# Optimization experiments

Measured on AMD Instinct MI355X. Metric: run time of the kernel, lower is better.

The kernel has to match this reference:

```python
import jax, jax.numpy as jnp
import numpy as np

NU, NI, D, H = 200000, 100000, 128, 128
E = 600000

def _segment_mean(vals, seg_ids, num_segments):
    s = jax.ops.segment_sum(vals, seg_ids, num_segments=num_segments)
    cnt = jax.ops.segment_sum(jnp.ones((vals.shape[0],), vals.dtype), seg_ids, num_segments=num_segments)
    return s / jnp.maximum(cnt, 1.0)[:, None]


def setup_inputs() -> dict:
    key = jax.random.key(0)
    ks = jax.random.split(key, 16)
    sc = 1.0 / np.sqrt(D)
    return {
        'x_user': jax.random.normal(ks[0], (NU, D), jnp.float32),
        'x_item': jax.random.normal(ks[1], (NI, D), jnp.float32),
        'edge_src_ui': jax.random.randint(ks[2], (E,), 0, NU),
        'edge_dst_ui': jax.random.randint(ks[3], (E,), 0, NI),
        'edge_src_iu': jax.random.randint(ks[4], (E,), 0, NI),
        'edge_dst_iu': jax.random.randint(ks[5], (E,), 0, NU),
        'Wl_ui': jax.random.normal(ks[6], (D, H), jnp.float32) * sc,
        'bl_ui': jax.random.normal(ks[7], (H,), jnp.float32) * 0.01,
        'Wr_ui': jax.random.normal(ks[8], (D, H), jnp.float32) * sc,
        'Wl_iu': jax.random.normal(ks[9], (D, H), jnp.float32) * sc,
        'bl_iu': jax.random.normal(ks[10], (H,), jnp.float32) * 0.01,
        'Wr_iu': jax.random.normal(ks[11], (D, H), jnp.float32) * sc,
        'W_user': jax.random.normal(ks[12], (H, H), jnp.float32) * sc,
        'b_user': jax.random.normal(ks[13], (H,), jnp.float32) * 0.01,
        'W_item': jax.random.normal(ks[14], (H, H), jnp.float32) * sc,
        'b_item': jax.random.normal(ks[15], (H,), jnp.float32) * 0.01,
    }


def reference(x_user, x_item, edge_src_ui, edge_dst_ui, edge_src_iu, edge_dst_iu,
              Wl_ui, bl_ui, Wr_ui, Wl_iu, bl_iu, Wr_iu,
              W_user, b_user, W_item, b_item):
    # SAGEConv per edge type: out_dst = mean_aggr(x_src[src]) @ Wl + bl + x_dst @ Wr
    agg_item = _segment_mean(x_user[edge_src_ui], edge_dst_ui, NI)   # [NI, D]
    h_item = agg_item @ Wl_ui + bl_ui + x_item @ Wr_ui               # [NI, H]
    agg_user = _segment_mean(x_item[edge_src_iu], edge_dst_iu, NU)   # [NU, D]
    h_user = agg_user @ Wl_iu + bl_iu + x_user @ Wr_iu               # [NU, H]
    # HeteroConv aggr='sum' is trivial here (one edge type per dst node type).
    out_user = jax.nn.relu(h_user @ W_user + b_user)
    out_item = jax.nn.relu(h_item @ W_item + b_item)
    return jnp.concatenate([out_user, out_item], axis=0)  # [NU+NI, H]
```

## Files before the change

kernel.cpp:

```cpp
#include <hip/hip_runtime.h>

#define NUu 200000
#define NIi 100000
#define EE  600000

#define SCAP 768
#define NB_USER 3125
#define NB_ITEM 1563

#define PB_HIST   586
#define PB_W0     1172
#define PB_B0     1428
#define PB_CU0    1429
#define PB_CI0    13929
#define PB_END    20179

typedef short short8 __attribute__((ext_vector_type(8)));
typedef float floatx4 __attribute__((ext_vector_type(4)));

__device__ __forceinline__ unsigned short f2bf(float f) {
  union { float f; unsigned int u; } v; v.f = f;
  unsigned int r = v.u + 0x7FFFu + ((v.u >> 16) & 1u);
  return (unsigned short)(r >> 16);
}
__device__ __forceinline__ float bflo(unsigned int u) { return __uint_as_float(u << 16); }
__device__ __forceinline__ float bfhi(unsigned int u) { return __uint_as_float(u & 0xFFFF0000u); }

__global__ __launch_bounds__(256) void prep(
    const int* __restrict__ edst_iu, int* __restrict__ cnt_user,
    const int* __restrict__ edst_ui, int* __restrict__ cnt_item,
    const float* __restrict__ Wl_iu, const float* __restrict__ Wr_iu,
    const float* __restrict__ Wl_ui, const float* __restrict__ Wr_ui,
    const float* __restrict__ W_user, const float* __restrict__ W_item,
    unsigned short* __restrict__ Wp_user, unsigned short* __restrict__ Wp_item,
    const float* __restrict__ bl_iu, const float* __restrict__ b_user,
    const float* __restrict__ bl_ui, const float* __restrict__ b_item,
    float* __restrict__ bias_user, float* __restrict__ bias_item,
    const float* __restrict__ x_user, const float* __restrict__ x_item,
    unsigned short* __restrict__ xb_user, unsigned short* __restrict__ xb_item)
{
  int b = blockIdx.x, t = threadIdx.x;
  if (b < PB_W0) {
    const int* edst = b < PB_HIST ? edst_iu : edst_ui;
    int* cnt        = b < PB_HIST ? cnt_user : cnt_item;
    int local       = b < PB_HIST ? b : b - PB_HIST;
    int idx = local * 1024 + t * 4;
    if (idx < EE) {
      int4 v = *(const int4*)(edst + idx);
      atomicAdd(&cnt[v.x], 1); atomicAdd(&cnt[v.y], 1);
      atomicAdd(&cnt[v.z], 1); atomicAdd(&cnt[v.w], 1);
    }
  } else if (b < PB_B0) {
    int flat = (b - PB_W0) * 256 + t;
    int h = flat & 127, d = (flat >> 7) & 127, m = flat >> 14;
    const float* A; const float* W; unsigned short* dst; int koff;
    switch (m) {
      case 0:  A = Wl_iu; W = W_user; dst = Wp_user; koff = 0;   break;
      case 1:  A = Wr_iu; W = W_user; dst = Wp_user; koff = 128; break;
      case 2:  A = Wl_ui; W = W_item; dst = Wp_item; koff = 0;   break;
      default: A = Wr_ui; W = W_item; dst = Wp_item; koff = 128; break;
    }
    float acc = 0.f;
    for (int k = 0; k < 128; ++k) acc += A[d * 128 + k] * W[k * 128 + h];
    int kg = koff + d;
    int ks = kg >> 5, quad = (kg >> 3) & 3, j = kg & 7;
    int nt = h >> 4, nlo = h & 15;
    dst[((nt * 8 + ks) * 64 + quad * 16 + nlo) * 8 + j] = f2bf(acc);
  } else if (b == PB_B0) {
    int pair = t >> 7, h = t & 127;
    const float* bl = pair ? bl_ui : bl_iu;
    const float* b2 = pair ? b_item : b_user;
    const float* W  = pair ? W_item : W_user;
    float* o        = pair ? bias_item : bias_user;
    float acc = b2[h];
    for (int k = 0; k < 128; ++k) acc += bl[k] * W[k * 128 + h];
    o[h] = acc;
  } else {
    const float* src; unsigned short* dst; long base;
    if (b < PB_CI0) { src = x_user; dst = xb_user; base = (long)(b - PB_CU0) * 2048 + t * 8; }
    else            { src = x_item; dst = xb_item; base = (long)(b - PB_CI0) * 2048 + t * 8; }
    const float4* p4 = (const float4*)(src + base);
    float4 lo = p4[0], hi = p4[1];
    uint4 p;
    p.x = (unsigned)f2bf(lo.x) | ((unsigned)f2bf(lo.y) << 16);
    p.y = (unsigned)f2bf(lo.z) | ((unsigned)f2bf(lo.w) << 16);
    p.z = (unsigned)f2bf(hi.x) | ((unsigned)f2bf(hi.y) << 16);
    p.w = (unsigned)f2bf(hi.z) | ((unsigned)f2bf(hi.w) << 16);
    *(uint4*)(dst + base) = p;
  }
}

__global__ __launch_bounds__(256) void scan1(
    const int* __restrict__ cnt_u, int* __restrict__ blk_u,
    const int* __restrict__ cnt_i, int* __restrict__ blk_i)
{
  __shared__ int s[256];
  int b = blockIdx.x, t = threadIdx.x;
  const int* cnt; int* blksum; int N;
  if (blockIdx.y == 0) { cnt = cnt_u; blksum = blk_u; N = NUu; }
  else { if (b >= 98) return; cnt = cnt_i; blksum = blk_i; N = NIi; }
  int base = b * 1024 + t * 4;
  int v = 0;
  #pragma unroll
  for (int j = 0; j < 4; ++j) { int i = base + j; if (i < N) v += cnt[i]; }
  s[t] = v; __syncthreads();
  for (int off = 128; off > 0; off >>= 1) {
    if (t < off) s[t] += s[t + off];
    __syncthreads();
  }
  if (t == 0) blksum[b] = s[0];
}

__global__ __launch_bounds__(256) void scan3(
    const int* __restrict__ cnt_u, const int* __restrict__ blks_u,
    int* __restrict__ row_u, int* __restrict__ fil_u,
    const int* __restrict__ cnt_i, const int* __restrict__ blks_i,
    int* __restrict__ row_i, int* __restrict__ fil_i)
{
  __shared__ int s[256];
  int b = blockIdx.x, t = threadIdx.x;
  const int* cnt; const int* blksum; int* rowp; int* fillp; int N; int nblk;
  if (blockIdx.y == 0) { cnt = cnt_u; blksum = blks_u; rowp = row_u; fillp = fil_u; N = NUu; nblk = 196; }
  else { if (b >= 98) return; cnt = cnt_i; blksum = blks_i; rowp = row_i; fillp = fil_i; N = NIi; nblk = 98; }

  int v2 = t < nblk ? blksum[t] : 0;
  s[t] = v2; __syncthreads();
  for (int off = 1; off < 256; off <<= 1) {
    int tmp = t >= off ? s[t - off] : 0;
    __syncthreads();
    s[t] += tmp;
    __syncthreads();
  }
  int blkoffb = (b == 0) ? 0 : s[b - 1];
  __syncthreads();

  int base = b * 1024 + t * 4;
  int v[4]; int sum = 0;
  #pragma unroll
  for (int j = 0; j < 4; ++j) { int i = base + j; v[j] = (i < N) ? cnt[i] : 0; sum += v[j]; }
  s[t] = sum; __syncthreads();
  for (int off = 1; off < 256; off <<= 1) {
    int tmp = t >= off ? s[t - off] : 0;
    __syncthreads();
    s[t] += tmp;
    __syncthreads();
  }
  int ex = s[t] - sum + blkoffb;
  #pragma unroll
  for (int j = 0; j < 4; ++j) {
    int i = base + j;
    if (i < N) { rowp[i] = ex; fillp[i] = ex; ex += v[j]; }
  }
}

__global__ __launch_bounds__(256) void fill2(
    const int* __restrict__ esrc_iu, const int* __restrict__ edst_iu,
    int* __restrict__ fill_user, int* __restrict__ srcs_user,
    const int* __restrict__ esrc_ui, const int* __restrict__ edst_ui,
    int* __restrict__ fill_item, int* __restrict__ srcs_item)
{
  int e = blockIdx.x * 256 + threadIdx.x;
  if (e >= EE) return;
  const int* esrc; const int* edst; int* fillp; int* srcs;
  if (blockIdx.y == 0) { esrc = esrc_iu; edst = edst_iu; fillp = fill_user; srcs = srcs_user; }
  else                 { esrc = esrc_ui; edst = edst_ui; fillp = fill_item; srcs = srcs_item; }
  int d = edst[e];
  int p = atomicAdd(&fillp[d], 1);
  srcs[p] = esrc[e];
}

template<bool BF>
__global__ __launch_bounds__(256, 8) void fused_gemm(
    const void* __restrict__ xu_own, const void* __restrict__ xu_src,
    const int* __restrict__ rowp_u, const int* __restrict__ srcs_u,
    const unsigned short* __restrict__ Wp_u, const float* __restrict__ bias_u,
    const void* __restrict__ xi_own, const void* __restrict__ xi_src,
    const int* __restrict__ rowp_i, const int* __restrict__ srcs_i,
    const unsigned short* __restrict__ Wp_i, const float* __restrict__ bias_i,
    float* __restrict__ out)
{
  __shared__ __align__(16) uint4 ldsA4[1024];
  __shared__ int ldsS[SCAP];
  __shared__ int rb[65];
  int t = threadIdx.x;
  int b = blockIdx.x;

  const void* xown; const void* xsrc; const int* rowp; const int* srcs;
  const unsigned short* Wp; const float* bias; float* outbase; int nvalid; int node0;
  if (b < NB_USER) {
    xown = xu_own; xsrc = xu_src; rowp = rowp_u; srcs = srcs_u;
    Wp = Wp_u; bias = bias_u; outbase = out; nvalid = NUu; node0 = b * 64;
  } else {
    xown = xi_own; xsrc = xi_src; rowp = rowp_i; srcs = srcs_i;
    Wp = Wp_i; bias = bias_i; outbase = out + (size_t)NUu * 128;
    nvalid = NIi; node0 = (b - NB_USER) * 64;
  }

  if (t < 65) {
    int node = node0 + t;
    rb[t] = node < nvalid ? rowp[node] : EE;
  }
  __syncthreads();
  int rs0 = rb[0];
  int W = rb[64] - rs0;
  for (int idx = t; idx < W && idx < SCAP; idx += 256)
    ldsS[idx] = srcs[rs0 + idx];

  #pragma unroll
  for (int i = 0; i < 4; ++i) {
    int oid = t + i * 256;
    int m = oid >> 4;
    int oct = oid & 15;
    int node = node0 + m;
    uint4 p; p.x = 0u; p.y = 0u; p.z = 0u; p.w = 0u;
    if (node < nvalid) {
      if constexpr (BF) {
        p = *(const uint4*)((const unsigned short*)xown + (size_t)node * 128 + oct * 8);
      } else {
        const float4* p4 = (const float4*)((const float*)xown + (size_t)node * 128 + oct * 8);
        float4 lo = p4[0], hi = p4[1];
        p.x = (unsigned)f2bf(lo.x) | ((unsigned)f2bf(lo.y) << 16);
        p.y = (unsigned)f2bf(lo.z) | ((unsigned)f2bf(lo.w) << 16);
        p.z = (unsigned)f2bf(hi.x) | ((unsigned)f2bf(hi.y) << 16);
        p.w = (unsigned)f2bf(hi.z) | ((unsigned)f2bf(hi.w) << 16);
      }
    }
    int ks = oct >> 2, quad = oct & 3;
    int mt = m >> 4, mlo = m & 15;
    ldsA4[(mt * 4 + ks) * 64 + quad * 16 + (mlo ^ (oct & 7))] = p;
  }
  __syncthreads();

  int wave = t >> 6, lane = t & 63;
  int quadr = lane >> 4, mlor = lane & 15;
  floatx4 acc[8];
  #pragma unroll
  for (int i = 0; i < 8; ++i) acc[i] = (floatx4){0.f, 0.f, 0.f, 0.f};
  const short8* A = (const short8*)ldsA4;
  const short8* B = (const short8*)Wp;
  #pragma unroll
  for (int kk = 0; kk < 4; ++kk) {
    short8 af = A[(wave * 4 + kk) * 64 + quadr * 16 + (mlor ^ ((kk * 4 + quadr) & 7))];
    #pragma unroll
    for (int nt = 0; nt < 8; ++nt) {
      short8 bf = B[(nt * 8 + 4 + kk) * 64 + lane];
      acc[nt] = __builtin_amdgcn_mfma_f32_16x16x32_bf16(af, bf, acc[nt], 0, 0, 0);
    }
  }
  __syncthreads();

  #pragma unroll
  for (int i = 0; i < 8; ++i) {
    int oid = t + i * 256;
    int m = oid >> 5;
    int oct = oid & 31;
    int slice = oct & 15;
    int par = oct >> 4;
    int node = node0 + m;
    float a0=0,a1=0,a2=0,a3=0,a4=0,a5=0,a6=0,a7=0;
    int deg = 0;
    if (node < nvalid) {
      int erel = rb[m] - rs0;
      deg = rb[m + 1] - rb[m];
      int k0 = slice * 8;
      int e = par;
      if constexpr (BF) {
        const unsigned short* xs = (const unsigned short*)xsrc;
        for (; e + 2 < deg; e += 4) {
          int q0 = erel + e, q1 = q0 + 2;
          int s0 = (q0 < SCAP) ? ldsS[q0] : srcs[rs0 + q0];
          int s1 = (q1 < SCAP) ? ldsS[q1] : srcs[rs0 + q1];
          uint4 v0 = *(const uint4*)(xs + (size_t)s0 * 128 + k0);
          uint4 v1 = *(const uint4*)(xs + (size_t)s1 * 128 + k0);
          a0 += bflo(v0.x) + bflo(v1.x); a1 += bfhi(v0.x) + bfhi(v1.x);
          a2 += bflo(v0.y) + bflo(v1.y); a3 += bfhi(v0.y) + bfhi(v1.y);
          a4 += bflo(v0.z) + bflo(v1.z); a5 += bfhi(v0.z) + bfhi(v1.z);
          a6 += bflo(v0.w) + bflo(v1.w); a7 += bfhi(v0.w) + bfhi(v1.w);
        }
        if (e < deg) {
          int q = erel + e;
          int s = (q < SCAP) ? ldsS[q] : srcs[rs0 + q];
          uint4 v0 = *(const uint4*)(xs + (size_t)s * 128 + k0);
          a0 += bflo(v0.x); a1 += bfhi(v0.x);
          a2 += bflo(v0.y); a3 += bfhi(v0.y);
          a4 += bflo(v0.z); a5 += bfhi(v0.z);
          a6 += bflo(v0.w); a7 += bfhi(v0.w);
        }
      } else {
        const float* xs = (const float*)xsrc;
        for (; e + 2 < deg; e += 4) {
          int q0 = erel + e, q1 = q0 + 2;
          int s0 = (q0 < SCAP) ? ldsS[q0] : srcs[rs0 + q0];
          int s1 = (q1 < SCAP) ? ldsS[q1] : srcs[rs0 + q1];
          const float4* r0 = (const float4*)(xs + (size_t)s0 * 128 + k0);
          const float4* r1 = (const float4*)(xs + (size_t)s1 * 128 + k0);
          float4 l0 = r0[0], h0 = r0[1];
          float4 l1 = r1[0], h1 = r1[1];
          a0 += l0.x + l1.x; a1 += l0.y + l1.y;
          a2 += l0.z + l1.z; a3 += l0.w + l1.w;
          a4 += h0.x + h1.x; a5 += h0.y + h1.y;
          a6 += h0.z + h1.z; a7 += h0.w + h1.w;
        }
        if (e < deg) {
          int q = erel + e;
          int s = (q < SCAP) ? ldsS[q] : srcs[rs0 + q];
          const float4* r = (const float4*)(xs + (size_t)s * 128 + k0);
          float4 l = r[0], h = r[1];
          a0 += l.x; a1 += l.y; a2 += l.z; a3 += l.w;
          a4 += h.x; a5 += h.y; a6 += h.z; a7 += h.w;
        }
      }
    }
    a0 += __shfl_xor(a0, 16); a1 += __shfl_xor(a1, 16);
    a2 += __shfl_xor(a2, 16); a3 += __shfl_xor(a3, 16);
    a4 += __shfl_xor(a4, 16); a5 += __shfl_xor(a5, 16);
    a6 += __shfl_xor(a6, 16); a7 += __shfl_xor(a7, 16);
    if (par == 0) {
      float sc = deg > 0 ? 1.0f / (float)deg : 0.f;
      uint4 p;
      p.x = (unsigned)f2bf(a0 * sc) | ((unsigned)f2bf(a1 * sc) << 16);
      p.y = (unsigned)f2bf(a2 * sc) | ((unsigned)f2bf(a3 * sc) << 16);
      p.z = (unsigned)f2bf(a4 * sc) | ((unsigned)f2bf(a5 * sc) << 16);
      p.w = (unsigned)f2bf(a6 * sc) | ((unsigned)f2bf(a7 * sc) << 16);
      int ks = slice >> 2, quad = slice & 3;
      int mt = m >> 4, mlo = m & 15;
      ldsA4[(mt * 4 + ks) * 64 + quad * 16 + (mlo ^ (slice & 7))] = p;
    }
  }
  __syncthreads();

  #pragma unroll
  for (int kk = 0; kk < 4; ++kk) {
    short8 af = A[(wave * 4 + kk) * 64 + quadr * 16 + (mlor ^ ((kk * 4 + quadr) & 7))];
    #pragma unroll
    for (int nt = 0; nt < 8; ++nt) {
      short8 bf = B[(nt * 8 + kk) * 64 + lane];
      acc[nt] = __builtin_amdgcn_mfma_f32_16x16x32_bf16(af, bf, acc[nt], 0, 0, 0);
    }
  }

  int col = lane & 15, qrow = (lane >> 4) * 4;
  #pragma unroll
  for (int nt = 0; nt < 8; ++nt) {
    int n = nt * 16 + col;
    float bv = bias[n];
    #pragma unroll
    for (int r2 = 0; r2 < 4; ++r2) {
      int node = node0 + wave * 16 + qrow + r2;
      if (node < nvalid) {
        float v = acc[nt][r2] + bv;
        v = v > 0.f ? v : 0.f;
        __builtin_nontemporal_store(v, &outbase[(size_t)node * 128 + n]);
      }
    }
  }
}

extern "C" void kernel_launch(void* const* d_in, const int* in_sizes, int n_in,
                              void* d_out, int out_size, void* d_ws, size_t ws_size,
                              hipStream_t stream)
{
  const float* x_user = (const float*)d_in[0];
  const float* x_item = (const float*)d_in[1];
  const int* esrc_ui  = (const int*)d_in[2];
  const int* edst_ui  = (const int*)d_in[3];
  const int* esrc_iu  = (const int*)d_in[4];
  const int* edst_iu  = (const int*)d_in[5];
  const float* Wl_ui  = (const float*)d_in[6];
  const float* bl_ui  = (const float*)d_in[7];
  const float* Wr_ui  = (const float*)d_in[8];
  const float* Wl_iu  = (const float*)d_in[9];
  const float* bl_iu  = (const float*)d_in[10];
  const float* Wr_iu  = (const float*)d_in[11];
  const float* W_user = (const float*)d_in[12];
  const float* b_user = (const float*)d_in[13];
  const float* W_item = (const float*)d_in[14];
  const float* b_item = (const float*)d_in[15];
  float* out = (float*)d_out;

  char* ws = (char*)d_ws;
  int* cnt_user  = (int*)(ws + 0);
  int* cnt_item  = (int*)(ws + 800000);
  int* row_user  = (int*)(ws + 1200000);
  int* row_item  = (int*)(ws + 2000000);
  int* fill_user = (int*)(ws + 2400000);
  int* fill_item = (int*)(ws + 3200000);
  int* srcs_user = (int*)(ws + 3600000);
  int* srcs_item = (int*)(ws + 6000000);
  int* blks_user = (int*)(ws + 8400000);
  int* blks_item = (int*)(ws + 8401024);
  unsigned short* Wp_user = (unsigned short*)(ws + 8404224);
  unsigned short* Wp_item = (unsigned short*)(ws + 8469760);
  float* bias_user = (float*)(ws + 8535296);
  float* bias_item = (float*)(ws + 8535808);
  unsigned short* xb_user = (unsigned short*)(ws + 8536320);
  unsigned short* xb_item = (unsigned short*)(ws + 59736320UL);

  const bool bf = ws_size >= 85336320UL;

  hipMemsetAsync(d_ws, 0, 1200000, stream);

  prep<<<bf ? PB_END : PB_CU0, 256, 0, stream>>>(
      edst_iu, cnt_user, edst_ui, cnt_item,
      Wl_iu, Wr_iu, Wl_ui, Wr_ui, W_user, W_item, Wp_user, Wp_item,
      bl_iu, b_user, bl_ui, b_item, bias_user, bias_item,
      x_user, x_item, xb_user, xb_item);

  scan1<<<dim3(196, 2), 256, 0, stream>>>(cnt_user, blks_user, cnt_item, blks_item);
  scan3<<<dim3(196, 2), 256, 0, stream>>>(cnt_user, blks_user, row_user, fill_user,
                                          cnt_item, blks_item, row_item, fill_item);

  const int EB = (EE + 255) / 256;
  fill2<<<dim3(EB, 2), 256, 0, stream>>>(esrc_iu, edst_iu, fill_user, srcs_user,
                                         esrc_ui, edst_ui, fill_item, srcs_item);

  if (bf) {
    fused_gemm<true><<<NB_USER + NB_ITEM, 256, 0, stream>>>(
        xb_user, xb_item, row_user, srcs_user, Wp_user, bias_user,
        xb_item, xb_user, row_item, srcs_item, Wp_item, bias_item, out);
  } else {
    fused_gemm<false><<<NB_USER + NB_ITEM, 256, 0, stream>>>(
        x_user, x_item, row_user, srcs_user, Wp_user, bias_user,
        x_item, x_user, row_item, srcs_item, Wp_item, bias_item, out);
  }
}
```

Baseline: 567.5 us.

## Replace global-atomic CSR build with two-level binned counting sort

Builds the CSR adjacency with a two-level counting sort instead of per-node global atomics. Destination nodes are grouped into bins of 512. Per-block shared-memory histograms are prefix-summed by a small kernel, edges are scattered into bin-ordered temporaries, and a per-bin kernel builds row pointers and the source list using shared-memory atomics. This removes the workspace memset and the contended global atomics in histogram and fill. The cost is an extra kernel, a serial 586-step loop per thread in the 2-block scan kernel, and extra temporary traffic.

Measured after the change: 684.2 us. 1.21x slower.

```diff
diff --git a/kernel.cpp b/kernel.cpp
--- a/kernel.cpp
+++ b/kernel.cpp
@@ -8,12 +8,17 @@
 #define NB_USER 3125
 #define NB_ITEM 1563
 
-#define PB_HIST   586
-#define PB_W0     1172
-#define PB_B0     1428
-#define PB_CU0    1429
-#define PB_CI0    13929
-#define PB_END    20179
+#define EB2 586
+#define NBIN 512
+#define BINS_U 391
+#define BINS_I 196
+
+#define PB_HIST 586
+#define PB_W0   1172
+#define PB_B0   1428
+#define PB_CU0  1429
+#define PB_CI0  13929
+#define PB_END  20179
 
 typedef short short8 __attribute__((ext_vector_type(8)));
 typedef float floatx4 __attribute__((ext_vector_type(4)));
@@ -26,9 +31,9 @@
 __device__ __forceinline__ float bflo(unsigned int u) { return __uint_as_float(u << 16); }
 __device__ __forceinline__ float bfhi(unsigned int u) { return __uint_as_float(u & 0xFFFF0000u); }
 
-__global__ __launch_bounds__(256) void prep(
-    const int* __restrict__ edst_iu, int* __restrict__ cnt_user,
-    const int* __restrict__ edst_ui, int* __restrict__ cnt_item,
+__global__ __launch_bounds__(256) void prep1(
+    const int* __restrict__ edst_iu, int* __restrict__ bh_u,
+    const int* __restrict__ edst_ui, int* __restrict__ bh_i,
     const float* __restrict__ Wl_iu, const float* __restrict__ Wr_iu,
     const float* __restrict__ Wl_ui, const float* __restrict__ Wr_ui,
     const float* __restrict__ W_user, const float* __restrict__ W_item,
@@ -39,20 +44,29 @@
     const float* __restrict__ x_user, const float* __restrict__ x_item,
     unsigned short* __restrict__ xb_user, unsigned short* __restrict__ xb_item)
 {
+  __shared__ int h[NBIN];
   int b = blockIdx.x, t = threadIdx.x;
   if (b < PB_W0) {
-    const int* edst = b < PB_HIST ? edst_iu : edst_ui;
-    int* cnt        = b < PB_HIST ? cnt_user : cnt_item;
-    int local       = b < PB_HIST ? b : b - PB_HIST;
-    int idx = local * 1024 + t * 4;
+    bool uside = b < PB_HIST;
+    const int* ed = uside ? edst_iu : edst_ui;
+    int* bh       = uside ? bh_u : bh_i;
+    int lb        = uside ? b : b - PB_HIST;
+    h[t] = 0; h[t + 256] = 0;
+    __syncthreads();
+    int idx = lb * 1024 + t * 4;
     if (idx < EE) {
-      int4 v = *(const int4*)(edst + idx);
-      atomicAdd(&cnt[v.x], 1); atomicAdd(&cnt[v.y], 1);
-      atomicAdd(&cnt[v.z], 1); atomicAdd(&cnt[v.w], 1);
-    }
+      int4 d = *(const int4*)(ed + idx);
+      atomicAdd(&h[d.x >> 9], 1);
+      atomicAdd(&h[d.y >> 9], 1);
+      atomicAdd(&h[d.z >> 9], 1);
+      atomicAdd(&h[d.w >> 9], 1);
+    }
+    __syncthreads();
+    bh[t * EB2 + lb] = h[t];
+    bh[(t + 256) * EB2 + lb] = h[t + 256];
   } else if (b < PB_B0) {
     int flat = (b - PB_W0) * 256 + t;
-    int h = flat & 127, d = (flat >> 7) & 127, m = flat >> 14;
+    int hh = flat & 127, d = (flat >> 7) & 127, m = flat >> 14;
     const float* A; const float* W; unsigned short* dst; int koff;
     switch (m) {
       case 0:  A = Wl_iu; W = W_user; dst = Wp_user; koff = 0;   break;
@@ -61,20 +75,20 @@
       default: A = Wr_ui; W = W_item; dst = Wp_item; koff = 128; break;
     }
     float acc = 0.f;
-    for (int k = 0; k < 128; ++k) acc += A[d * 128 + k] * W[k * 128 + h];
+    for (int k = 0; k < 128; ++k) acc += A[d * 128 + k] * W[k * 128 + hh];
     int kg = koff + d;
     int ks = kg >> 5, quad = (kg >> 3) & 3, j = kg & 7;
-    int nt = h >> 4, nlo = h & 15;
+    int nt = hh >> 4, nlo = hh & 15;
     dst[((nt * 8 + ks) * 64 + quad * 16 + nlo) * 8 + j] = f2bf(acc);
   } else if (b == PB_B0) {
-    int pair = t >> 7, h = t & 127;
+    int pair = t >> 7, hh = t & 127;
     const float* bl = pair ? bl_ui : bl_iu;
     const float* b2 = pair ? b_item : b_user;
     const float* W  = pair ? W_item : W_user;
     float* o        = pair ? bias_item : bias_user;
-    float acc = b2[h];
-    for (int k = 0; k < 128; ++k) acc += bl[k] * W[k * 128 + h];
-    o[h] = acc;
+    float acc = b2[hh];
+    for (int k = 0; k < 128; ++k) acc += bl[k] * W[k * 128 + hh];
+    o[hh] = acc;
   } else {
     const float* src; unsigned short* dst; long base;
     if (b < PB_CI0) { src = x_user; dst = xb_user; base = (long)(b - PB_CU0) * 2048 + t * 8; }
@@ -90,83 +104,114 @@
   }
 }
 
-__global__ __launch_bounds__(256) void scan1(
-    const int* __restrict__ cnt_u, int* __restrict__ blk_u,
-    const int* __restrict__ cnt_i, int* __restrict__ blk_i)
-{
-  __shared__ int s[256];
+__global__ __launch_bounds__(512) void prep2(
+    int* __restrict__ bh_u, int* __restrict__ bb_u,
+    int* __restrict__ bh_i, int* __restrict__ bb_i)
+{
+  __shared__ int s[512];
+  int side = blockIdx.x, t = threadIdx.x;
+  int* bh = side ? bh_i : bh_u;
+  int* bb = side ? bb_i : bb_u;
+  int rowbase = t * EB2;
+  int tot = 0;
+  for (int b = 0; b < EB2; ++b) tot += bh[rowbase + b];
+  s[t] = tot; __syncthreads();
+  for (int off = 1; off < 512; off <<= 1) {
+    int v = t >= off ? s[t - off] : 0;
+    __syncthreads();
+    s[t] += v;
+    __syncthreads();
+  }
+  int base = t ? s[t - 1] : 0;
+  bb[t] = base;
+  if (t == 511) bb[512] = s[511];
+  int run = base;
+  for (int b = 0; b < EB2; ++b) {
+    int v = bh[rowbase + b];
+    bh[rowbase + b] = run;
+    run += v;
+  }
+}
+
+__global__ __launch_bounds__(256) void prep3(
+    const int* __restrict__ esrc_iu, const int* __restrict__ edst_iu,
+    const int* __restrict__ bh_u, int2* __restrict__ tmp_u,
+    const int* __restrict__ esrc_ui, const int* __restrict__ edst_ui,
+    const int* __restrict__ bh_i, int2* __restrict__ tmp_i)
+{
+  __shared__ int ofl[NBIN];
+  __shared__ int rk[NBIN];
   int b = blockIdx.x, t = threadIdx.x;
-  const int* cnt; int* blksum; int N;
-  if (blockIdx.y == 0) { cnt = cnt_u; blksum = blk_u; N = NUu; }
-  else { if (b >= 98) return; cnt = cnt_i; blksum = blk_i; N = NIi; }
-  int base = b * 1024 + t * 4;
-  int v = 0;
-  #pragma unroll
-  for (int j = 0; j < 4; ++j) { int i = base + j; if (i < N) v += cnt[i]; }
-  s[t] = v; __syncthreads();
-  for (int off = 128; off > 0; off >>= 1) {
-    if (t < off) s[t] += s[t + off];
-    __syncthreads();
-  }
-  if (t == 0) blksum[b] = s[0];
-}
-
-__global__ __launch_bounds__(256) void scan3(
-    const int* __restrict__ cnt_u, const int* __restrict__ blks_u,
-    int* __restrict__ row_u, int* __restrict__ fil_u,
-    const int* __restrict__ cnt_i, const int* __restrict__ blks_i,
-    int* __restrict__ row_i, int* __restrict__ fil_i)
-{
-  __shared__ int s[256];
-  int b = blockIdx.x, t = threadIdx.x;
-  const int* cnt; const int* blksum; int* rowp; int* fillp; int N; int nblk;
-  if (blockIdx.y == 0) { cnt = cnt_u; blksum = blks_u; rowp = row_u; fillp = fil_u; N = NUu; nblk = 196; }
-  else { if (b >= 98) return; cnt = cnt_i; blksum = blks_i; rowp = row_i; fillp = fil_i; N = NIi; nblk = 98; }
-
-  int v2 = t < nblk ? blksum[t] : 0;
-  s[t] = v2; __syncthreads();
-  for (int off = 1; off < 256; off <<= 1) {
-    int tmp = t >= off ? s[t - off] : 0;
-    __syncthreads();
-    s[t] += tmp;
-    __syncthreads();
-  }
-  int blkoffb = (b == 0) ? 0 : s[b - 1];
-  __syncthreads();
-
-  int base = b * 1024 + t * 4;
-  int v[4]; int sum = 0;
-  #pragma unroll
-  for (int j = 0; j < 4; ++j) { int i = base + j; v[j] = (i < N) ? cnt[i] : 0; sum += v[j]; }
-  s[t] = sum; __syncthreads();
-  for (int off = 1; off < 256; off <<= 1) {
-    int tmp = t >= off ? s[t - off] : 0;
-    __syncthreads();
-    s[t] += tmp;
-    __syncthreads();
-  }
-  int ex = s[t] - sum + blkoffb;
-  #pragma unroll
-  for (int j = 0; j < 4; ++j) {
-    int i = base + j;
-    if (i < N) { rowp[i] = ex; fillp[i] = ex; ex += v[j]; }
-  }
-}
-
-__global__ __launch_bounds__(256) void fill2(
-    const int* __restrict__ esrc_iu, const int* __restrict__ edst_iu,
-    int* __restrict__ fill_user, int* __restrict__ srcs_user,
-    const int* __restrict__ esrc_ui, const int* __restrict__ edst_ui,
-    int* __restrict__ fill_item, int* __restrict__ srcs_item)
-{
-  int e = blockIdx.x * 256 + threadIdx.x;
-  if (e >= EE) return;
-  const int* esrc; const int* edst; int* fillp; int* srcs;
-  if (blockIdx.y == 0) { esrc = esrc_iu; edst = edst_iu; fillp = fill_user; srcs = srcs_user; }
-  else                 { esrc = esrc_ui; edst = edst_ui; fillp = fill_item; srcs = srcs_item; }
-  int d = edst[e];
-  int p = atomicAdd(&fillp[d], 1);
-  srcs[p] = esrc[e];
+  bool uside = blockIdx.y == 0;
+  const int* es = uside ? esrc_iu : esrc_ui;
+  const int* ed = uside ? edst_iu : edst_ui;
+  const int* bh = uside ? bh_u : bh_i;
+  int2* tmp     = uside ? tmp_u : tmp_i;
+  ofl[t] = bh[t * EB2 + b];
+  ofl[t + 256] = bh[(t + 256) * EB2 + b];
+  rk[t] = 0; rk[t + 256] = 0;
+  __syncthreads();
+  int idx = b * 1024 + t * 4;
+  if (idx < EE) {
+    int4 s4 = *(const int4*)(es + idx);
+    int4 d4 = *(const int4*)(ed + idx);
+    int bn, r;
+    bn = d4.x >> 9; r = atomicAdd(&rk[bn], 1); tmp[ofl[bn] + r] = make_int2(s4.x, d4.x);
+    bn = d4.y >> 9; r = atomicAdd(&rk[bn], 1); tmp[ofl[bn] + r] = make_int2(s4.y, d4.y);
+    bn = d4.z >> 9; r = atomicAdd(&rk[bn], 1); tmp[ofl[bn] + r] = make_int2(s4.z, d4.z);
+    bn = d4.w >> 9; r = atomicAdd(&rk[bn], 1); tmp[ofl[bn] + r] = make_int2(s4.w, d4.w);
+  }
+}
+
+__global__ __launch_bounds__(256) void prep4(
+    const int2* __restrict__ tmp_u, const int* __restrict__ bb_u,
+    int* __restrict__ row_u, int* __restrict__ srcs_u,
+    const int2* __restrict__ tmp_i, const int* __restrict__ bb_i,
+    int* __restrict__ row_i, int* __restrict__ srcs_i)
+{
+  int bin = blockIdx.x, t = threadIdx.x;
+  bool uside = blockIdx.y == 0;
+  int nbins = uside ? BINS_U : BINS_I;
+  if (bin >= nbins) return;
+  int N = uside ? NUu : NIi;
+  const int2* tmp = uside ? tmp_u : tmp_i;
+  const int* bb   = uside ? bb_u : bb_i;
+  int* rowp       = uside ? row_u : row_i;
+  int* srcs       = uside ? srcs_u : srcs_i;
+  int ebase = bb[bin], eend = bb[bin + 1];
+  int node0 = bin << 9;
+
+  __shared__ int cnt[512];
+  __shared__ int off[512];
+  __shared__ int s1[256];
+  cnt[t] = 0; cnt[t + 256] = 0;
+  __syncthreads();
+  for (int e = ebase + t; e < eend; e += 256)
+    atomicAdd(&cnt[tmp[e].y - node0], 1);
+  __syncthreads();
+  int a = cnt[2 * t], b2 = cnt[2 * t + 1];
+  s1[t] = a + b2; __syncthreads();
+  for (int o = 1; o < 256; o <<= 1) {
+    int v = t >= o ? s1[t - o] : 0;
+    __syncthreads();
+    s1[t] += v;
+    __syncthreads();
+  }
+  int base = t ? s1[t - 1] : 0;
+  off[2 * t] = base;
+  off[2 * t + 1] = base + a;
+  __syncthreads();
+  int nloc = N - node0; if (nloc > 512) nloc = 512;
+  if (t < nloc)       rowp[node0 + t]       = ebase + off[t];
+  if (t + 256 < nloc) rowp[node0 + t + 256] = ebase + off[t + 256];
+  cnt[t] = 0; cnt[t + 256] = 0;
+  __syncthreads();
+  for (int e = ebase + t; e < eend; e += 256) {
+    int2 p = tmp[e];
+    int l = p.y - node0;
+    int r = atomicAdd(&cnt[l], 1);
+    srcs[ebase + off[l] + r] = p.x;
+  }
 }
 
 template<bool BF>
@@ -379,40 +424,40 @@
   float* out = (float*)d_out;
 
   char* ws = (char*)d_ws;
-  int* cnt_user  = (int*)(ws + 0);
-  int* cnt_item  = (int*)(ws + 800000);
-  int* row_user  = (int*)(ws + 1200000);
-  int* row_item  = (int*)(ws + 2000000);
-  int* fill_user = (int*)(ws + 2400000);
-  int* fill_item = (int*)(ws + 3200000);
-  int* srcs_user = (int*)(ws + 3600000);
-  int* srcs_item = (int*)(ws + 6000000);
-  int* blks_user = (int*)(ws + 8400000);
-  int* blks_item = (int*)(ws + 8401024);
-  unsigned short* Wp_user = (unsigned short*)(ws + 8404224);
-  unsigned short* Wp_item = (unsigned short*)(ws + 8469760);
-  float* bias_user = (float*)(ws + 8535296);
-  float* bias_item = (float*)(ws + 8535808);
-  unsigned short* xb_user = (unsigned short*)(ws + 8536320);
-  unsigned short* xb_item = (unsigned short*)(ws + 59736320UL);
-
-  const bool bf = ws_size >= 85336320UL;
-
-  hipMemsetAsync(d_ws, 0, 1200000, stream);
-
-  prep<<<bf ? PB_END : PB_CU0, 256, 0, stream>>>(
-      edst_iu, cnt_user, edst_ui, cnt_item,
+  int* bh_u      = (int*)(ws + 0);
+  int* bh_i      = (int*)(ws + 1200128);
+  int* bb_u      = (int*)(ws + 2400256);
+  int* bb_i      = (int*)(ws + 2402308);
+  int2* tmp_u    = (int2*)(ws + 2404864);
+  int2* tmp_i    = (int2*)(ws + 7204864);
+  int* row_user  = (int*)(ws + 12004864UL);
+  int* row_item  = (int*)(ws + 12804864UL);
+  int* srcs_user = (int*)(ws + 13204864UL);
+  int* srcs_item = (int*)(ws + 15604864UL);
+  unsigned short* Wp_user = (unsigned short*)(ws + 18004864UL);
+  unsigned short* Wp_item = (unsigned short*)(ws + 18070400UL);
+  float* bias_user = (float*)(ws + 18135936UL);
+  float* bias_item = (float*)(ws + 18136448UL);
+  unsigned short* xb_user = (unsigned short*)(ws + 18136960UL);
+  unsigned short* xb_item = (unsigned short*)(ws + 69336960UL);
+
+  const bool bf = ws_size >= 94936960UL;
+
+  prep1<<<bf ? PB_END : PB_CU0, 256, 0, stream>>>(
+      edst_iu, bh_u, edst_ui, bh_i,
       Wl_iu, Wr_iu, Wl_ui, Wr_ui, W_user, W_item, Wp_user, Wp_item,
       bl_iu, b_user, bl_ui, b_item, bias_user, bias_item,
       x_user, x_item, xb_user, xb_item);
 
-  scan1<<<dim3(196, 2), 256, 0, stream>>>(cnt_user, blks_user, cnt_item, blks_item);
-  scan3<<<dim3(196, 2), 256, 0, stream>>>(cnt_user, blks_user, row_user, fill_user,
-                                          cnt_item, blks_item, row_item, fill_item);
-
-  const int EB = (EE + 255) / 256;
-  fill2<<<dim3(EB, 2), 256, 0, stream>>>(esrc_iu, edst_iu, fill_user, srcs_user,
-                                         esrc_ui, edst_ui, fill_item, srcs_item);
+  prep2<<<2, 512, 0, stream>>>(bh_u, bb_u, bh_i, bb_i);
+
+  prep3<<<dim3(EB2, 2), 256, 0, stream>>>(
+      esrc_iu, edst_iu, bh_u, tmp_u,
+      esrc_ui, edst_ui, bh_i, tmp_i);
+
+  prep4<<<dim3(BINS_U, 2), 256, 0, stream>>>(
+      tmp_u, bb_u, row_user, srcs_user,
+      tmp_i, bb_i, row_item, srcs_item);
 
   if (bf) {
     fused_gemm<true><<<NB_USER + NB_ITEM, 256, 0, stream>>>(
```
